# Performance work log

Measured on AMD Instinct MI355X. Metric: run time of the kernel, lower is better.

Reference implementation:

```python
import jax, jax.numpy as jnp
import numpy as np

NUM_USERS = 100000
NUM_ITEMS = 50000
NUM_EDGES = 4000000
DIM = 64


def setup_inputs() -> dict:
    key = jax.random.key(0)
    k1, k2, k3, k4, k5 = jax.random.split(key, 5)
    user_emb = jax.random.normal(k1, (NUM_USERS, DIM), dtype=jnp.float32)
    item_emb = jax.random.normal(k2, (NUM_ITEMS, DIM), dtype=jnp.float32)
    edge_norm = jax.random.uniform(k3, (NUM_EDGES,), dtype=jnp.float32)
    u_idx = jax.random.randint(k4, (NUM_EDGES,), 0, NUM_USERS, dtype=jnp.int32)
    i_idx = jax.random.randint(k5, (NUM_EDGES,), 0, NUM_ITEMS, dtype=jnp.int32)
    return {"user_emb": user_emb, "item_emb": item_emb, "edge_norm": edge_norm,
            "u_idx": u_idx, "i_idx": i_idx}


def reference(user_emb, item_emb, edge_norm, u_idx, i_idx):
    norm = edge_norm[:, None]  # [E, 1]
    # user -> item propagation
    msg_to_items = norm * user_emb[u_idx]  # [E, D]
    agg_items = jax.ops.segment_sum(msg_to_items, i_idx, num_segments=NUM_ITEMS)
    # item -> user propagation
    msg_to_users = norm * item_emb[i_idx]  # [E, D]
    agg_users = jax.ops.segment_sum(msg_to_users, u_idx, num_segments=NUM_USERS)
    return (agg_users, agg_items)
```

## Files before the change

### kernel.cpp

```cpp
#include <hip/hip_runtime.h>

#define NUM_USERS 100000
#define NUM_ITEMS 50000
#define NUM_EDGES 4000000
#define DIM 64

#define SLICE_SHIFT 15
#define SLICES_U ((NUM_USERS + (1 << SLICE_SHIFT) - 1) >> SLICE_SHIFT)
#define SLICES_I ((NUM_ITEMS + (1 << SLICE_SHIFT) - 1) >> SLICE_SHIFT)

#define N_I (SLICES_U * NUM_ITEMS)
#define N_U (SLICES_I * NUM_USERS)
#define N_TOTAL (N_I + N_U)

#define SCAN_NB 512
#define SCAN_THREADS 256

#define PCHUNK 4096
#define PWG ((NUM_EDGES + PCHUNK - 1) / PCHUNK)
#define BUK_SHIFT 9
#define NBUK_I ((N_I + 511) >> 9)
#define NBUK_U ((N_U + 511) >> 9)
#define NBUK (NBUK_I + NBUK_U)

#define STAGE_CAP 15360

#define W_SCALE 32767.0f
#define W_INV   (1.0f / 32767.0f)

__global__ __launch_bounds__(256) void lightgcn_scatter(
    const float* __restrict__ user_emb,
    const float* __restrict__ item_emb,
    const float* __restrict__ edge_norm,
    const int* __restrict__ u_idx,
    const int* __restrict__ i_idx,
    float* __restrict__ agg_users,
    float* __restrict__ agg_items)
{
    long long gid = (long long)blockIdx.x * blockDim.x + threadIdx.x;
    int edge = (int)(gid >> 6);
    int lane = (int)(gid & 63);
    if (edge >= NUM_EDGES) return;
    int u = u_idx[edge];
    int i = i_idx[edge];
    float n = edge_norm[edge];
    float uval = user_emb[(size_t)u * DIM + lane];
    float ival = item_emb[(size_t)i * DIM + lane];
    atomicAdd(&agg_items[(size_t)i * DIM + lane], n * uval);
    atomicAdd(&agg_users[(size_t)u * DIM + lane], n * ival);
}

__global__ __launch_bounds__(256) void convert_both(
    const float4* __restrict__ usrc, const float4* __restrict__ isrc,
    ushort4* __restrict__ udst, ushort4* __restrict__ idst,
    int un4, int in4)
{
    int t = blockIdx.x * blockDim.x + threadIdx.x;
    const float4* s; ushort4* d; int idx;
    if (t < un4) { s = usrc; d = udst; idx = t; }
    else if (t < un4 + in4) { s = isrc; d = idst; idx = t - un4; }
    else return;
    float4 v = s[idx];
    ushort4 o;
    uint b;
    b = __float_as_uint(v.x); o.x = (ushort)((b + 0x7FFFu + ((b >> 16) & 1u)) >> 16);
    b = __float_as_uint(v.y); o.y = (ushort)((b + 0x7FFFu + ((b >> 16) & 1u)) >> 16);
    b = __float_as_uint(v.z); o.z = (ushort)((b + 0x7FFFu + ((b >> 16) & 1u)) >> 16);
    b = __float_as_uint(v.w); o.w = (ushort)((b + 0x7FFFu + ((b >> 16) & 1u)) >> 16);
    d[idx] = o;
}

__global__ __launch_bounds__(256) void bucket_hist_conv(
    const int* __restrict__ u_idx, const int* __restrict__ i_idx,
    ushort* __restrict__ wgHist,
    const float4* __restrict__ usrc, const float4* __restrict__ isrc,
    ushort4* __restrict__ udst, ushort4* __restrict__ idst,
    int un4, int in4, int hist_blocks)
{
    __shared__ uint hist[NBUK];
    if ((int)blockIdx.x >= hist_blocks) {
        int ct = (blockIdx.x - hist_blocks) * blockDim.x + threadIdx.x;
        const float4* s; ushort4* d; int idx;
        if (ct < un4) { s = usrc; d = udst; idx = ct; }
        else if (ct < un4 + in4) { s = isrc; d = idst; idx = ct - un4; }
        else return;
        float4 v = s[idx];
        ushort4 o;
        uint b;
        b = __float_as_uint(v.x); o.x = (ushort)((b + 0x7FFFu + ((b >> 16) & 1u)) >> 16);
        b = __float_as_uint(v.y); o.y = (ushort)((b + 0x7FFFu + ((b >> 16) & 1u)) >> 16);
        b = __float_as_uint(v.z); o.z = (ushort)((b + 0x7FFFu + ((b >> 16) & 1u)) >> 16);
        b = __float_as_uint(v.w); o.w = (ushort)((b + 0x7FFFu + ((b >> 16) & 1u)) >> 16);
        d[idx] = o;
        return;
    }
    int t = threadIdx.x;
    for (int b = t; b < NBUK; b += 256) hist[b] = 0;
    __syncthreads();
    int e0 = blockIdx.x * PCHUNK;
    int ecnt = NUM_EDGES - e0; if (ecnt > PCHUNK) ecnt = PCHUNK;
    for (int k = t; k < ecnt; k += 256) {
        int u = u_idx[e0 + k];
        int i = i_idx[e0 + k];
        atomicAdd(&hist[((u >> SLICE_SHIFT) * NUM_ITEMS + i) >> BUK_SHIFT], 1u);
        atomicAdd(&hist[NBUK_I + (((i >> SLICE_SHIFT) * NUM_USERS + u) >> BUK_SHIFT)], 1u);
    }
    __syncthreads();
    ushort* row = wgHist + (size_t)blockIdx.x * NBUK;
    for (int b = t; b < NBUK; b += 256) row[b] = (ushort)hist[b];
}

__global__ __launch_bounds__(256) void mscan(
    const ushort* __restrict__ wgHist, uint* __restrict__ wgPrefixT,
    int* __restrict__ bukTot)
{
    __shared__ uint sm[256];
    int b = blockIdx.x, t = threadIdx.x;
    int i0 = t * 4;
    uint c0 = 0, c1 = 0, c2 = 0, c3 = 0;
    if (i0 + 0 < PWG) c0 = wgHist[(size_t)(i0 + 0) * NBUK + b];
    if (i0 + 1 < PWG) c1 = wgHist[(size_t)(i0 + 1) * NBUK + b];
    if (i0 + 2 < PWG) c2 = wgHist[(size_t)(i0 + 2) * NBUK + b];
    if (i0 + 3 < PWG) c3 = wgHist[(size_t)(i0 + 3) * NBUK + b];
    sm[t] = c0 + c1 + c2 + c3;
    __syncthreads();
    for (int o = 1; o < 256; o <<= 1) {
        uint x = (t >= o) ? sm[t - o] : 0;
        __syncthreads();
        sm[t] += x;
        __syncthreads();
    }
    uint excl = (t == 0) ? 0u : sm[t - 1];
    uint* orow = wgPrefixT + (size_t)b * PWG;
    if (i0 + 0 < PWG) orow[i0 + 0] = excl;
    if (i0 + 1 < PWG) orow[i0 + 1] = excl + c0;
    if (i0 + 2 < PWG) orow[i0 + 2] = excl + c0 + c1;
    if (i0 + 3 < PWG) orow[i0 + 3] = excl + c0 + c1 + c2;
    if (t == 255) bukTot[b] = (int)sm[255];
}

__global__ __launch_bounds__(256) void bucket_scan(
    const int* __restrict__ bukTot, int* __restrict__ bukOff,
    int* __restrict__ off_last)
{
    __shared__ int sm[256];
    int t = threadIdx.x;
    int b4 = t * 4;
    int v0 = 0, v1 = 0, v2 = 0, v3 = 0;
    if (b4 + 0 < NBUK) v0 = bukTot[b4 + 0];
    if (b4 + 1 < NBUK) v1 = bukTot[b4 + 1];
    if (b4 + 2 < NBUK) v2 = bukTot[b4 + 2];
    if (b4 + 3 < NBUK) v3 = bukTot[b4 + 3];
    sm[t] = v0 + v1 + v2 + v3;
    __syncthreads();
    for (int o = 1; o < 256; o <<= 1) {
        int x = (t >= o) ? sm[t - o] : 0;
        __syncthreads();
        sm[t] += x;
        __syncthreads();
    }
    int excl = (t == 0) ? 0 : sm[t - 1];
    if (b4 + 0 < NBUK) bukOff[b4 + 0] = excl;
    if (b4 + 1 < NBUK) bukOff[b4 + 1] = excl + v0;
    if (b4 + 2 < NBUK) bukOff[b4 + 2] = excl + v0 + v1;
    if (b4 + 3 < NBUK) bukOff[b4 + 3] = excl + v0 + v1 + v2;
    if (t == 255) bukOff[NBUK] = sm[255];
    if (t == 0) *off_last = 2 * NUM_EDGES;
}

__global__ __launch_bounds__(256) void partition_pairs(
    const int* __restrict__ u_idx, const int* __restrict__ i_idx,
    const float* __restrict__ edge_norm,
    const ushort* __restrict__ wgHist, const uint* __restrict__ wgPrefixT,
    const int* __restrict__ bukOff,
    uint* __restrict__ pairRec, ushort* __restrict__ pairBin)
{
    __shared__ uint recS[2 * PCHUNK];
    __shared__ uint bbS[2 * PCHUNK];
    __shared__ uint hist[NBUK];
    __shared__ uint cursor[NBUK];
    __shared__ uint gbase[NBUK];
    __shared__ uint scanTmp[256];

    int t  = threadIdx.x;
    int wg = blockIdx.x;
    int e0 = wg * PCHUNK;
    int ecnt = NUM_EDGES - e0; if (ecnt > PCHUNK) ecnt = PCHUNK;

    const ushort* hrow = wgHist + (size_t)wg * NBUK;
    for (int b = t; b < NBUK; b += 256) {
        hist[b]  = hrow[b];
        gbase[b] = (uint)bukOff[b] + wgPrefixT[(size_t)b * PWG + wg];
    }
    __syncthreads();

    int base4 = t * 4;
    uint v0 = 0, v1 = 0, v2 = 0, v3 = 0;
    if (base4 + 0 < NBUK) v0 = hist[base4 + 0];
    if (base4 + 1 < NBUK) v1 = hist[base4 + 1];
    if (base4 + 2 < NBUK) v2 = hist[base4 + 2];
    if (base4 + 3 < NBUK) v3 = hist[base4 + 3];
    scanTmp[t] = v0 + v1 + v2 + v3;
    __syncthreads();
    for (int o = 1; o < 256; o <<= 1) {
        uint x = (t >= o) ? scanTmp[t - o] : 0;
        __syncthreads();
        scanTmp[t] += x;
        __syncthreads();
    }
    uint excl = (t == 0) ? 0u : scanTmp[t - 1];
    if (base4 + 0 < NBUK) cursor[base4 + 0] = excl;
    if (base4 + 1 < NBUK) cursor[base4 + 1] = excl + v0;
    if (base4 + 2 < NBUK) cursor[base4 + 2] = excl + v0 + v1;
    if (base4 + 3 < NBUK) cursor[base4 + 3] = excl + v0 + v1 + v2;
    __syncthreads();

    for (int k = t; k < ecnt; k += 256) {
        int u = u_idx[e0 + k];
        int i = i_idx[e0 + k];
        float n = edge_norm[e0 + k];
        uint w = (uint)(n * W_SCALE + 0.5f); if (w > 32767u) w = 32767u;
        int binI = (u >> SLICE_SHIFT) * NUM_ITEMS + i;
        int binU = (i >> SLICE_SHIFT) * NUM_USERS + u;
        uint bI = (uint)(binI >> BUK_SHIFT);
        uint bU = (uint)(NBUK_I + (binU >> BUK_SHIFT));
        uint rI = atomicAdd(&cursor[bI], 1u);
        recS[rI] = ((uint)u << 15) | w;
        bbS[rI]  = (bI << BUK_SHIFT) | (uint)(binI & 511);
        uint rU = atomicAdd(&cursor[bU], 1u);
        recS[rU] = ((uint)i << 15) | w;
        bbS[rU]  = (bU << BUK_SHIFT) | (uint)(binU & 511);
    }
    __syncthreads();

    int total = 2 * ecnt;
    for (int s = t; s < total; s += 256) {
        uint bb = bbS[s];
        uint b  = bb >> BUK_SHIFT;
        uint wb = cursor[b] - hist[b];
        uint lpos = gbase[b] + ((uint)s - wb);
        pairRec[lpos] = recS[s];
        pairBin[lpos] = (ushort)(bb & 511u);
    }
}

__global__ __launch_bounds__(256) void bucket_fill(
    const int* __restrict__ bukOff,
    const uint* __restrict__ pairRec, const ushort* __restrict__ pairBin,
    int* __restrict__ off, uint* __restrict__ rec)
{
    __shared__ uint recS[STAGE_CAP];
    __shared__ uint lcnt[512];
    __shared__ uint cur[512];
    __shared__ uint scanTmp[256];
    int b = blockIdx.x, t = threadIdx.x;
    lcnt[t] = 0; lcnt[t + 256] = 0;
    __syncthreads();
    int s0 = bukOff[b], s1 = bukOff[b + 1];
    int n = s1 - s0;
    for (int k = t; k < n; k += 256)
        atomicAdd(&lcnt[pairBin[s0 + k]], 1u);
    __syncthreads();
    uint a0 = lcnt[2 * t], a1 = lcnt[2 * t + 1];
    scanTmp[t] = a0 + a1;
    __syncthreads();
    for (int o = 1; o < 256; o <<= 1) {
        uint x = (t >= o) ? scanTmp[t - o] : 0;
        __syncthreads();
        scanTmp[t] += x;
        __syncthreads();
    }
    uint excl = (t == 0) ? 0u : scanTmp[t - 1];
    cur[2 * t]     = excl;
    cur[2 * t + 1] = excl + a0;
    __syncthreads();
    int gbin0, dirEnd;
    if (b < NBUK_I) { gbin0 = b << BUK_SHIFT; dirEnd = N_I; }
    else { gbin0 = N_I + ((b - NBUK_I) << BUK_SHIFT); dirEnd = N_TOTAL; }
    int lim = dirEnd - gbin0; if (lim > 512) lim = 512;
    if (2 * t     < lim) off[gbin0 + 2 * t]     = s0 + (int)cur[2 * t];
    if (2 * t + 1 < lim) off[gbin0 + 2 * t + 1] = s0 + (int)cur[2 * t + 1];
    __syncthreads();
    if (n <= STAGE_CAP) {
        for (int k = t; k < n; k += 256) {
            uint lbin = pairBin[s0 + k];
            uint r = atomicAdd(&cur[lbin], 1u);
            recS[r] = pairRec[s0 + k];
        }
        __syncthreads();
        for (int k = t; k < n; k += 256)
            rec[(size_t)s0 + k] = recS[k];
    } else {
        for (int k = t; k < n; k += 256) {
            uint lbin = pairBin[s0 + k];
            uint r = atomicAdd(&cur[lbin], 1u);
            rec[(size_t)s0 + r] = pairRec[s0 + k];
        }
    }
}

__global__ __launch_bounds__(SCAN_THREADS) void scan_block_sums(
    const int* __restrict__ cnt, int* __restrict__ bsum, int n, int chunk)
{
    int b = blockIdx.x, t = threadIdx.x;
    int base = b * chunk;
    int end  = base + chunk < n ? base + chunk : n;
    int tch  = (chunk + SCAN_THREADS - 1) / SCAN_THREADS;
    int s = base + t * tch;
    int e = s + tch < end ? s + tch : end;
    int local = 0;
    for (int i = s; i < e; ++i) local += cnt[i];
    __shared__ int sm[SCAN_THREADS];
    sm[t] = local;
    __syncthreads();
    for (int o = SCAN_THREADS / 2; o > 0; o >>= 1) {
        if (t < o) sm[t] += sm[t + o];
        __syncthreads();
    }
    if (t == 0) bsum[b] = sm[0];
}

__global__ __launch_bounds__(SCAN_NB) void scan_block_offsets(
    const int* __restrict__ bsum, int* __restrict__ boff,
    int* __restrict__ off_end)
{
    int t = threadIdx.x;
    __shared__ int sm[SCAN_NB];
    int v = bsum[t];
    sm[t] = v;
    __syncthreads();
    for (int o = 1; o < SCAN_NB; o <<= 1) {
        int x = (t >= o) ? sm[t - o] : 0;
        __syncthreads();
        sm[t] += x;
        __syncthreads();
    }
    boff[t] = sm[t] - v;
    if (t == SCAN_NB - 1) *off_end = sm[SCAN_NB - 1];
}

__global__ __launch_bounds__(SCAN_THREADS) void scan_local(
    int* __restrict__ cnt, const int* __restrict__ boff, int n, int chunk)
{
    int b = blockIdx.x, t = threadIdx.x;
    int base = b * chunk;
    int end  = base + chunk < n ? base + chunk : n;
    int tch  = (chunk + SCAN_THREADS - 1) / SCAN_THREADS;
    int s = base + t * tch;
    int e = s + tch < end ? s + tch : end;
    int local = 0;
    for (int i = s; i < e; ++i) local += cnt[i];
    __shared__ int sm[SCAN_THREADS];
    sm[t] = local;
    __syncthreads();
    for (int o = 1; o < SCAN_THREADS; o <<= 1) {
        int x = (t >= o) ? sm[t - o] : 0;
        __syncthreads();
        sm[t] += x;
        __syncthreads();
    }
    int run = boff[b] + ((t == 0) ? 0 : sm[t - 1]);
    for (int i = s; i < e; ++i) {
        int c = cnt[i];
        cnt[i] = run;
        run += c;
    }
}

__global__ __launch_bounds__(256) void rank_both_exact(
    const int4* __restrict__ u4, const int4* __restrict__ i4,
    int* __restrict__ cnt, int n_i, int su_shift, int si_shift,
    int4* __restrict__ rank_i, int4* __restrict__ rank_u)
{
    int t = blockIdx.x * blockDim.x + threadIdx.x;
    if (t >= NUM_EDGES / 4) return;
    int4 u = u4[t];
    int4 i = i4[t];
    int4 ri, ru;
    ri.x = atomicAdd(&cnt[(u.x >> su_shift) * NUM_ITEMS + i.x], 1);
    ri.y = atomicAdd(&cnt[(u.y >> su_shift) * NUM_ITEMS + i.y], 1);
    ri.z = atomicAdd(&cnt[(u.z >> su_shift) * NUM_ITEMS + i.z], 1);
    ri.w = atomicAdd(&cnt[(u.w >> su_shift) * NUM_ITEMS + i.w], 1);
    ru.x = atomicAdd(&cnt[n_i + (i.x >> si_shift) * NUM_USERS + u.x], 1);
    ru.y = atomicAdd(&cnt[n_i + (i.y >> si_shift) * NUM_USERS + u.y], 1);
    ru.z = atomicAdd(&cnt[n_i + (i.z >> si_shift) * NUM_USERS + u.z], 1);
    ru.w = atomicAdd(&cnt[n_i + (i.w >> si_shift) * NUM_USERS + u.w], 1);
    rank_i[t] = ri;
    rank_u[t] = ru;
}

__global__ __launch_bounds__(256) void scatter_all(
    const int4* __restrict__ u4, const int4* __restrict__ i4,
    const float4* __restrict__ n4,
    const int4* __restrict__ rank_i, const int4* __restrict__ rank_u,
    const int* __restrict__ off, int n_i, int su_shift, int si_shift,
    uint* __restrict__ rec)
{
    int t = blockIdx.x * blockDim.x + threadIdx.x;
    if (t >= NUM_EDGES / 4) return;
    int4   u  = u4[t];
    int4   i  = i4[t];
    float4 n  = n4[t];
    int4   ri = rank_i[t];
    int4   ru = rank_u[t];
    uint w0 = (uint)(n.x * W_SCALE + 0.5f); if (w0 > 32767u) w0 = 32767u;
    uint w1 = (uint)(n.y * W_SCALE + 0.5f); if (w1 > 32767u) w1 = 32767u;
    uint w2 = (uint)(n.z * W_SCALE + 0.5f); if (w2 > 32767u) w2 = 32767u;
    uint w3 = (uint)(n.w * W_SCALE + 0.5f); if (w3 > 32767u) w3 = 32767u;
    int pi0 = off[(u.x >> su_shift) * NUM_ITEMS + i.x] + ri.x;
    int pi1 = off[(u.y >> su_shift) * NUM_ITEMS + i.y] + ri.y;
    int pi2 = off[(u.z >> su_shift) * NUM_ITEMS + i.z] + ri.z;
    int pi3 = off[(u.w >> su_shift) * NUM_ITEMS + i.w] + ri.w;
    int pu0 = off[n_i + (i.x >> si_shift) * NUM_USERS + u.x] + ru.x;
    int pu1 = off[n_i + (i.y >> si_shift) * NUM_USERS + u.y] + ru.y;
    int pu2 = off[n_i + (i.z >> si_shift) * NUM_USERS + u.z] + ru.z;
    int pu3 = off[n_i + (i.w >> si_shift) * NUM_USERS + u.w] + ru.w;
    rec[pi0] = ((uint)u.x << 15) | w0;
    rec[pi1] = ((uint)u.y << 15) | w1;
    rec[pi2] = ((uint)u.z << 15) | w2;
    rec[pi3] = ((uint)u.w << 15) | w3;
    rec[pu0] = ((uint)i.x << 15) | w0;
    rec[pu1] = ((uint)i.y << 15) | w1;
    rec[pu2] = ((uint)i.z << 15) | w2;
    rec[pu3] = ((uint)i.w << 15) | w3;
}

__global__ __launch_bounds__(256) void gather_pass(
    const int* __restrict__ off, int bin_base,
    const uint* __restrict__ rec,
    const ushort* __restrict__ emb16,
    float* __restrict__ out, int nrows, int accumulate)
{
    int gid  = blockIdx.x * blockDim.x + threadIdx.x;
    int row  = gid >> 6;
    int lane = gid & 63;
    if (row >= nrows) return;
    int b = bin_base + row;
    int s = off[b];
    int e = off[b + 1];
    float acc = accumulate ? out[(size_t)row * DIM + lane] : 0.f;
    int k = s;
    for (; k + 8 <= e; k += 8) {
        uint r0 = rec[k],   r1 = rec[k+1], r2 = rec[k+2], r3 = rec[k+3];
        uint r4 = rec[k+4], r5 = rec[k+5], r6 = rec[k+6], r7 = rec[k+7];
        ushort b0 = emb16[(size_t)(r0 >> 15) * DIM + lane];
        ushort b1 = emb16[(size_t)(r1 >> 15) * DIM + lane];
        ushort b2 = emb16[(size_t)(r2 >> 15) * DIM + lane];
        ushort b3 = emb16[(size_t)(r3 >> 15) * DIM + lane];
        ushort b4 = emb16[(size_t)(r4 >> 15) * DIM + lane];
        ushort b5 = emb16[(size_t)(r5 >> 15) * DIM + lane];
        ushort b6 = emb16[(size_t)(r6 >> 15) * DIM + lane];
        ushort b7 = emb16[(size_t)(r7 >> 15) * DIM + lane];
        acc += (float)(r0 & 0x7FFFu) * W_INV * __uint_as_float((uint)b0 << 16);
        acc += (float)(r1 & 0x7FFFu) * W_INV * __uint_as_float((uint)b1 << 16);
        acc += (float)(r2 & 0x7FFFu) * W_INV * __uint_as_float((uint)b2 << 16);
        acc += (float)(r3 & 0x7FFFu) * W_INV * __uint_as_float((uint)b3 << 16);
        acc += (float)(r4 & 0x7FFFu) * W_INV * __uint_as_float((uint)b4 << 16);
        acc += (float)(r5 & 0x7FFFu) * W_INV * __uint_as_float((uint)b5 << 16);
        acc += (float)(r6 & 0x7FFFu) * W_INV * __uint_as_float((uint)b6 << 16);
        acc += (float)(r7 & 0x7FFFu) * W_INV * __uint_as_float((uint)b7 << 16);
    }
    for (; k + 4 <= e; k += 4) {
        uint r0 = rec[k], r1 = rec[k+1], r2 = rec[k+2], r3 = rec[k+3];
        ushort b0 = emb16[(size_t)(r0 >> 15) * DIM + lane];
        ushort b1 = emb16[(size_t)(r1 >> 15) * DIM + lane];
        ushort b2 = emb16[(size_t)(r2 >> 15) * DIM + lane];
        ushort b3 = emb16[(size_t)(r3 >> 15) * DIM + lane];
        acc += (float)(r0 & 0x7FFFu) * W_INV * __uint_as_float((uint)b0 << 16);
        acc += (float)(r1 & 0x7FFFu) * W_INV * __uint_as_float((uint)b1 << 16);
        acc += (float)(r2 & 0x7FFFu) * W_INV * __uint_as_float((uint)b2 << 16);
        acc += (float)(r3 & 0x7FFFu) * W_INV * __uint_as_float((uint)b3 << 16);
    }
    for (; k < e; ++k) {
        uint r0 = rec[k];
        ushort b0 = emb16[(size_t)(r0 >> 15) * DIM + lane];
        acc += (float)(r0 & 0x7FFFu) * W_INV * __uint_as_float((uint)b0 << 16);
    }
    out[(size_t)row * DIM + lane] = acc;
}

extern "C" void kernel_launch(void* const* d_in, const int* in_sizes, int n_in,
                              void* d_out, int out_size, void* d_ws, size_t ws_size,
                              hipStream_t stream) {
    const float* user_emb  = (const float*)d_in[0];
    const float* item_emb  = (const float*)d_in[1];
    const float* edge_norm = (const float*)d_in[2];
    const int*   u_idx     = (const int*)d_in[3];
    const int*   i_idx     = (const int*)d_in[4];

    float* agg_users = (float*)d_out;
    float* agg_items = agg_users + (size_t)NUM_USERS * DIM;

    const int un4 = NUM_USERS * DIM / 4;
    const int in4 = NUM_ITEMS * DIM / 4;
    const int eb4 = (NUM_EDGES / 4 + 255) / 256;
    const int cb  = (un4 + in4 + 255) / 256;
    const size_t bf16_bytes = ((size_t)NUM_USERS + NUM_ITEMS) * DIM * sizeof(ushort);

    {
        const size_t off_bytes  = (size_t)(N_TOTAL + 1) * sizeof(int);
        const size_t buk_bytes  = (size_t)(2 * NBUK + 2) * sizeof(int);
        const size_t wgh_bytes  = (size_t)PWG * NBUK * sizeof(ushort);
        const size_t wgp_bytes  = (size_t)NBUK * PWG * sizeof(uint);
        const size_t prec_bytes = (size_t)2 * NUM_EDGES * sizeof(uint);
        const size_t pbin_bytes = (size_t)2 * NUM_EDGES * sizeof(ushort);
        const size_t rec_bytes  = (size_t)2 * NUM_EDGES * sizeof(uint);
        const size_t need = off_bytes + buk_bytes + 64 + wgh_bytes + 64
                          + wgp_bytes + 64 + prec_bytes + 64 + pbin_bytes + 64
                          + rec_bytes + 64 + bf16_bytes + 256;
        if (ws_size >= need) {
            char* p = (char*)d_ws;
            int*    off     = (int*)p;    p += off_bytes;
            int*    bukTot  = (int*)p;    p += (size_t)NBUK * sizeof(int);
            int*    bukOff  = (int*)p;    p += (size_t)(NBUK + 1) * sizeof(int);
            p = (char*)(((uintptr_t)p + 63) & ~(uintptr_t)63);
            ushort* wgHist  = (ushort*)p; p += wgh_bytes;
            p = (char*)(((uintptr_t)p + 63) & ~(uintptr_t)63);
            uint*   wgPrefixT = (uint*)p; p += wgp_bytes;
            p = (char*)(((uintptr_t)p + 63) & ~(uintptr_t)63);
            uint*   pairRec = (uint*)p;   p += prec_bytes;
            p = (char*)(((uintptr_t)p + 63) & ~(uintptr_t)63);
            ushort* pairBin = (ushort*)p; p += pbin_bytes;
            p = (char*)(((uintptr_t)p + 63) & ~(uintptr_t)63);
            uint*   rec     = (uint*)p;   p += rec_bytes;
            p = (char*)(((uintptr_t)p + 63) & ~(uintptr_t)63);
            ushort* ue16    = (ushort*)p; p += (size_t)NUM_USERS * DIM * sizeof(ushort);
            ushort* ie16    = (ushort*)p;

            bucket_hist_conv<<<PWG + cb, 256, 0, stream>>>(
                u_idx, i_idx, wgHist,
                (const float4*)user_emb, (const float4*)item_emb,
                (ushort4*)ue16, (ushort4*)ie16, un4, in4, PWG);
            mscan<<<NBUK, 256, 0, stream>>>(wgHist, wgPrefixT, bukTot);
            bucket_scan<<<1, 256, 0, stream>>>(bukTot, bukOff, off + N_TOTAL);
            partition_pairs<<<PWG, 256, 0, stream>>>(
                u_idx, i_idx, edge_norm, wgHist, wgPrefixT, bukOff,
                pairRec, pairBin);
            bucket_fill<<<NBUK, 256, 0, stream>>>(
                bukOff, pairRec, pairBin, off, rec);
            for (int s = 0; s < SLICES_U; ++s) {
                gather_pass<<<((NUM_ITEMS * 64) + 255) / 256, 256, 0, stream>>>(
                    off, s * NUM_ITEMS, rec, ue16, agg_items, NUM_ITEMS,
                    s > 0 ? 1 : 0);
            }
            for (int s = 0; s < SLICES_I; ++s) {
                gather_pass<<<((NUM_USERS * 64) + 255) / 256, 256, 0, stream>>>(
                    off, N_I + s * NUM_USERS, rec, ie16, agg_users, NUM_USERS,
                    s > 0 ? 1 : 0);
            }
            return;
        }
    }

    {
        const size_t rec_bytes  = (size_t)2 * NUM_EDGES * sizeof(uint);
        const size_t rank_bytes = (size_t)2 * NUM_EDGES * sizeof(int);
        auto need_for = [&](int SU, int SI) -> size_t {
            size_t n_total = (size_t)SU * NUM_ITEMS + (size_t)SI * NUM_USERS;
            size_t off_bytes = (n_total + 1 + 2 * SCAN_NB) * sizeof(int);
            return off_bytes + 64 + rec_bytes + 64 + rank_bytes + 64 + bf16_bytes
                 + 256;
        };
        int SU = 0, SI = 0, su_shift = 17, si_shift = 17;
        if (ws_size >= need_for(SLICES_U, SLICES_I)) {
            SU = SLICES_U; SI = SLICES_I;
            su_shift = SLICE_SHIFT; si_shift = SLICE_SHIFT;
        } else if (ws_size >= need_for(1, 1)) {
            SU = 1; SI = 1;
        }
        if (SU > 0) {
            const int n_i = SU * NUM_ITEMS;
            const int n_u = SI * NUM_USERS;
            const int n_total = n_i + n_u;

            char* p = (char*)d_ws;
            int*   cnt  = (int*)p;   p += (size_t)(n_total + 1) * sizeof(int);
            int*   bsum = (int*)p;   p += (size_t)SCAN_NB * sizeof(int);
            int*   boff = (int*)p;   p += (size_t)SCAN_NB * sizeof(int);
            p = (char*)(((uintptr_t)p + 63) & ~(uintptr_t)63);
            uint*  rec  = (uint*)p;  p += rec_bytes;
            p = (char*)(((uintptr_t)p + 63) & ~(uintptr_t)63);
            int*   rank_i = (int*)p; p += (size_t)NUM_EDGES * sizeof(int);
            int*   rank_u = (int*)p; p += (size_t)NUM_EDGES * sizeof(int);
            p = (char*)(((uintptr_t)p + 63) & ~(uintptr_t)63);
            ushort* ue16 = (ushort*)p; p += (size_t)NUM_USERS * DIM * sizeof(ushort);
            ushort* ie16 = (ushort*)p;

            hipMemsetAsync(cnt, 0, (size_t)(n_total + 1) * sizeof(int), stream);
            convert_both<<<cb, 256, 0, stream>>>(
                (const float4*)user_emb, (const float4*)item_emb,
                (ushort4*)ue16, (ushort4*)ie16, un4, in4);
            rank_both_exact<<<eb4, 256, 0, stream>>>(
                (const int4*)u_idx, (const int4*)i_idx, cnt, n_i,
                su_shift, si_shift, (int4*)rank_i, (int4*)rank_u);
            const int chunk = (n_total + SCAN_NB - 1) / SCAN_NB;
            scan_block_sums<<<SCAN_NB, SCAN_THREADS, 0, stream>>>(
                cnt, bsum, n_total, chunk);
            scan_block_offsets<<<1, SCAN_NB, 0, stream>>>(bsum, boff, cnt + n_total);
            scan_local<<<SCAN_NB, SCAN_THREADS, 0, stream>>>(
                cnt, boff, n_total, chunk);
            scatter_all<<<eb4, 256, 0, stream>>>(
                (const int4*)u_idx, (const int4*)i_idx, (const float4*)edge_norm,
                (const int4*)rank_i, (const int4*)rank_u,
                cnt, n_i, su_shift, si_shift, rec);
            for (int s = 0; s < SU; ++s) {
                gather_pass<<<((NUM_ITEMS * 64) + 255) / 256, 256, 0, stream>>>(
                    cnt, s * NUM_ITEMS, rec, ue16, agg_items, NUM_ITEMS,
                    s > 0 ? 1 : 0);
            }
            for (int s = 0; s < SI; ++s) {
                gather_pass<<<((NUM_USERS * 64) + 255) / 256, 256, 0, stream>>>(
                    cnt, n_i + s * NUM_USERS, rec, ie16, agg_users, NUM_USERS,
                    s > 0 ? 1 : 0);
            }
            return;
        }
    }

    hipMemsetAsync(d_out, 0, (size_t)out_size * sizeof(float), stream);
    const long long total_threads = (long long)NUM_EDGES * 64;
    const int blocks = (int)((total_threads + 255) / 256);
    lightgcn_scatter<<<blocks, 256, 0, stream>>>(
        user_emb, item_emb, edge_norm, u_idx, i_idx, agg_users, agg_items);
}
```

Measured before the change: 471.7 us.

## Fuse per-slice gather passes into one kernel; widen bucket_fill to 512 threads

The separate gather_pass launches (one per slice per direction, some doing read-modify-write on the output) become a single gather_all kernel. Each output row walks all of its slice spans in registers and writes once, with the inner loop unrolled by 8. bucket_fill now runs one thread per bin with 512 threads, so its scan covers 512 entries directly. This removes repeated output read-modify-write traffic and several kernel launches, at the cost of a longer scan and possibly lower occupancy in bucket_fill.

```diff
diff --git a/kernel.cpp b/kernel.cpp
--- a/kernel.cpp
+++ b/kernel.cpp
@@ -24,6 +24,7 @@
 #define NBUK (NBUK_I + NBUK_U)
 
 #define STAGE_CAP 15360
+#define BF_THREADS 512
 
 #define W_SCALE 32767.0f
 #define W_INV   (1.0f / 32767.0f)
@@ -244,59 +245,119 @@
     }
 }
 
-__global__ __launch_bounds__(256) void bucket_fill(
+__global__ __launch_bounds__(BF_THREADS) void bucket_fill(
     const int* __restrict__ bukOff,
     const uint* __restrict__ pairRec, const ushort* __restrict__ pairBin,
     int* __restrict__ off, uint* __restrict__ rec)
 {
     __shared__ uint recS[STAGE_CAP];
     __shared__ uint lcnt[512];
+    __shared__ uint scanSm[512];
     __shared__ uint cur[512];
-    __shared__ uint scanTmp[256];
     int b = blockIdx.x, t = threadIdx.x;
-    lcnt[t] = 0; lcnt[t + 256] = 0;
+    lcnt[t] = 0;
     __syncthreads();
     int s0 = bukOff[b], s1 = bukOff[b + 1];
     int n = s1 - s0;
-    for (int k = t; k < n; k += 256)
+    for (int k = t; k < n; k += BF_THREADS)
         atomicAdd(&lcnt[pairBin[s0 + k]], 1u);
     __syncthreads();
-    uint a0 = lcnt[2 * t], a1 = lcnt[2 * t + 1];
-    scanTmp[t] = a0 + a1;
-    __syncthreads();
-    for (int o = 1; o < 256; o <<= 1) {
-        uint x = (t >= o) ? scanTmp[t - o] : 0;
-        __syncthreads();
-        scanTmp[t] += x;
-        __syncthreads();
-    }
-    uint excl = (t == 0) ? 0u : scanTmp[t - 1];
-    cur[2 * t]     = excl;
-    cur[2 * t + 1] = excl + a0;
-    __syncthreads();
+    uint v = lcnt[t];
+    scanSm[t] = v;
+    __syncthreads();
+    for (int o = 1; o < 512; o <<= 1) {
+        uint x = (t >= o) ? scanSm[t - o] : 0;
+        __syncthreads();
+        scanSm[t] += x;
+        __syncthreads();
+    }
+    uint excl = scanSm[t] - v;
+    cur[t] = excl;
     int gbin0, dirEnd;
     if (b < NBUK_I) { gbin0 = b << BUK_SHIFT; dirEnd = N_I; }
     else { gbin0 = N_I + ((b - NBUK_I) << BUK_SHIFT); dirEnd = N_TOTAL; }
     int lim = dirEnd - gbin0; if (lim > 512) lim = 512;
-    if (2 * t     < lim) off[gbin0 + 2 * t]     = s0 + (int)cur[2 * t];
-    if (2 * t + 1 < lim) off[gbin0 + 2 * t + 1] = s0 + (int)cur[2 * t + 1];
+    if (t < lim) off[gbin0 + t] = s0 + (int)excl;
     __syncthreads();
     if (n <= STAGE_CAP) {
-        for (int k = t; k < n; k += 256) {
+        for (int k = t; k < n; k += BF_THREADS) {
             uint lbin = pairBin[s0 + k];
             uint r = atomicAdd(&cur[lbin], 1u);
             recS[r] = pairRec[s0 + k];
         }
         __syncthreads();
-        for (int k = t; k < n; k += 256)
+        for (int k = t; k < n; k += BF_THREADS)
             rec[(size_t)s0 + k] = recS[k];
     } else {
-        for (int k = t; k < n; k += 256) {
+        for (int k = t; k < n; k += BF_THREADS) {
             uint lbin = pairBin[s0 + k];
             uint r = atomicAdd(&cur[lbin], 1u);
             rec[(size_t)s0 + r] = pairRec[s0 + k];
         }
     }
+}
+
+__global__ __launch_bounds__(256) void gather_all(
+    const int* __restrict__ off, const uint* __restrict__ rec,
+    const ushort* __restrict__ ue16, const ushort* __restrict__ ie16,
+    float* __restrict__ agg_users, float* __restrict__ agg_items)
+{
+    int gid  = blockIdx.x * blockDim.x + threadIdx.x;
+    int row  = gid >> 6;
+    int lane = gid & 63;
+    if (row >= NUM_ITEMS + NUM_USERS) return;
+    const ushort* emb; float* outp; int nspans, bin0, binStride;
+    if (row < NUM_ITEMS) {
+        emb = ue16; outp = agg_items + (size_t)row * DIM;
+        nspans = SLICES_U; bin0 = row; binStride = NUM_ITEMS;
+    } else {
+        int r = row - NUM_ITEMS;
+        emb = ie16; outp = agg_users + (size_t)r * DIM;
+        nspans = SLICES_I; bin0 = N_I + r; binStride = NUM_USERS;
+    }
+    float acc = 0.f;
+    for (int sp = 0; sp < nspans; ++sp) {
+        int bidx = bin0 + sp * binStride;
+        int k = off[bidx];
+        int e = off[bidx + 1];
+        for (; k + 8 <= e; k += 8) {
+            uint r0 = rec[k],   r1 = rec[k+1], r2 = rec[k+2], r3 = rec[k+3];
+            uint r4 = rec[k+4], r5 = rec[k+5], r6 = rec[k+6], r7 = rec[k+7];
+            ushort b0 = emb[(size_t)(r0 >> 15) * DIM + lane];
+            ushort b1 = emb[(size_t)(r1 >> 15) * DIM + lane];
+            ushort b2 = emb[(size_t)(r2 >> 15) * DIM + lane];
+            ushort b3 = emb[(size_t)(r3 >> 15) * DIM + lane];
+            ushort b4 = emb[(size_t)(r4 >> 15) * DIM + lane];
+            ushort b5 = emb[(size_t)(r5 >> 15) * DIM + lane];
+            ushort b6 = emb[(size_t)(r6 >> 15) * DIM + lane];
+            ushort b7 = emb[(size_t)(r7 >> 15) * DIM + lane];
+            acc += (float)(r0 & 0x7FFFu) * W_INV * __uint_as_float((uint)b0 << 16);
+            acc += (float)(r1 & 0x7FFFu) * W_INV * __uint_as_float((uint)b1 << 16);
+            acc += (float)(r2 & 0x7FFFu) * W_INV * __uint_as_float((uint)b2 << 16);
+            acc += (float)(r3 & 0x7FFFu) * W_INV * __uint_as_float((uint)b3 << 16);
+            acc += (float)(r4 & 0x7FFFu) * W_INV * __uint_as_float((uint)b4 << 16);
+            acc += (float)(r5 & 0x7FFFu) * W_INV * __uint_as_float((uint)b5 << 16);
+            acc += (float)(r6 & 0x7FFFu) * W_INV * __uint_as_float((uint)b6 << 16);
+            acc += (float)(r7 & 0x7FFFu) * W_INV * __uint_as_float((uint)b7 << 16);
+        }
+        for (; k + 4 <= e; k += 4) {
+            uint r0 = rec[k], r1 = rec[k+1], r2 = rec[k+2], r3 = rec[k+3];
+            ushort b0 = emb[(size_t)(r0 >> 15) * DIM + lane];
+            ushort b1 = emb[(size_t)(r1 >> 15) * DIM + lane];
+            ushort b2 = emb[(size_t)(r2 >> 15) * DIM + lane];
+            ushort b3 = emb[(size_t)(r3 >> 15) * DIM + lane];
+            acc += (float)(r0 & 0x7FFFu) * W_INV * __uint_as_float((uint)b0 << 16);
+            acc += (float)(r1 & 0x7FFFu) * W_INV * __uint_as_float((uint)b1 << 16);
+            acc += (float)(r2 & 0x7FFFu) * W_INV * __uint_as_float((uint)b2 << 16);
+            acc += (float)(r3 & 0x7FFFu) * W_INV * __uint_as_float((uint)b3 << 16);
+        }
+        for (; k < e; ++k) {
+            uint r0 = rec[k];
+            ushort b0 = emb[(size_t)(r0 >> 15) * DIM + lane];
+            acc += (float)(r0 & 0x7FFFu) * W_INV * __uint_as_float((uint)b0 << 16);
+        }
+    }
+    outp[lane] = acc;
 }
 
 __global__ __launch_bounds__(SCAN_THREADS) void scan_block_sums(
@@ -536,18 +597,11 @@
             partition_pairs<<<PWG, 256, 0, stream>>>(
                 u_idx, i_idx, edge_norm, wgHist, wgPrefixT, bukOff,
                 pairRec, pairBin);
-            bucket_fill<<<NBUK, 256, 0, stream>>>(
+            bucket_fill<<<NBUK, BF_THREADS, 0, stream>>>(
                 bukOff, pairRec, pairBin, off, rec);
-            for (int s = 0; s < SLICES_U; ++s) {
-                gather_pass<<<((NUM_ITEMS * 64) + 255) / 256, 256, 0, stream>>>(
-                    off, s * NUM_ITEMS, rec, ue16, agg_items, NUM_ITEMS,
-                    s > 0 ? 1 : 0);
-            }
-            for (int s = 0; s < SLICES_I; ++s) {
-                gather_pass<<<((NUM_USERS * 64) + 255) / 256, 256, 0, stream>>>(
-                    off, N_I + s * NUM_USERS, rec, ie16, agg_users, NUM_USERS,
-                    s > 0 ? 1 : 0);
-            }
+            const int grows = NUM_ITEMS + NUM_USERS;
+            gather_all<<<((grows * 64) + 255) / 256, 256, 0, stream>>>(
+                off, rec, ue16, ie16, agg_users, agg_items);
             return;
         }
     }
```

After: 435.8 us. 1.08x faster.

## Fuse per-slice gather passes into one multi-row kernel with finer slices and larger buckets

Applied to the files above, without the earlier changes.

Replaces the per-slice gather_pass launches with a single gather_dir kernel per direction. Each wavefront keeps 16 output rows in registers and loops over all slices, so partial sums are no longer reread and rewritten in global memory between passes. The slice width drops to 2^14 rows so each slice's embedding window is smaller and more cache-friendly, and buckets grow to 1024 bins with 512-thread bucket_fill blocks. The risks are fewer waves in the gather kernels, register pressure from the 16-entry accumulator array, and buckets that more often overflow the shared staging capacity.

```diff
diff --git a/kernel.cpp b/kernel.cpp
--- a/kernel.cpp
+++ b/kernel.cpp
@@ -5,7 +5,7 @@
 #define NUM_EDGES 4000000
 #define DIM 64
 
-#define SLICE_SHIFT 15
+#define SLICE_SHIFT 14
 #define SLICES_U ((NUM_USERS + (1 << SLICE_SHIFT) - 1) >> SLICE_SHIFT)
 #define SLICES_I ((NUM_ITEMS + (1 << SLICE_SHIFT) - 1) >> SLICE_SHIFT)
 
@@ -18,12 +18,16 @@
 
 #define PCHUNK 4096
 #define PWG ((NUM_EDGES + PCHUNK - 1) / PCHUNK)
-#define BUK_SHIFT 9
-#define NBUK_I ((N_I + 511) >> 9)
-#define NBUK_U ((N_U + 511) >> 9)
+#define BUK_SHIFT 10
+#define BUK_BINS (1 << BUK_SHIFT)
+#define NBUK_I ((N_I + BUK_BINS - 1) >> BUK_SHIFT)
+#define NBUK_U ((N_U + BUK_BINS - 1) >> BUK_SHIFT)
 #define NBUK (NBUK_I + NBUK_U)
 
 #define STAGE_CAP 15360
+#define BF_THREADS 512
+
+#define GW_ROWS 16
 
 #define W_SCALE 32767.0f
 #define W_INV   (1.0f / 32767.0f)
@@ -226,10 +230,10 @@
         uint bU = (uint)(NBUK_I + (binU >> BUK_SHIFT));
         uint rI = atomicAdd(&cursor[bI], 1u);
         recS[rI] = ((uint)u << 15) | w;
-        bbS[rI]  = (bI << BUK_SHIFT) | (uint)(binI & 511);
+        bbS[rI]  = (bI << BUK_SHIFT) | (uint)(binI & (BUK_BINS - 1));
         uint rU = atomicAdd(&cursor[bU], 1u);
         recS[rU] = ((uint)i << 15) | w;
-        bbS[rU]  = (bU << BUK_SHIFT) | (uint)(binU & 511);
+        bbS[rU]  = (bU << BUK_SHIFT) | (uint)(binU & (BUK_BINS - 1));
     }
     __syncthreads();
 
@@ -240,62 +244,128 @@
         uint wb = cursor[b] - hist[b];
         uint lpos = gbase[b] + ((uint)s - wb);
         pairRec[lpos] = recS[s];
-        pairBin[lpos] = (ushort)(bb & 511u);
-    }
-}
-
-__global__ __launch_bounds__(256) void bucket_fill(
+        pairBin[lpos] = (ushort)(bb & (BUK_BINS - 1));
+    }
+}
+
+__global__ __launch_bounds__(BF_THREADS) void bucket_fill(
     const int* __restrict__ bukOff,
     const uint* __restrict__ pairRec, const ushort* __restrict__ pairBin,
     int* __restrict__ off, uint* __restrict__ rec)
 {
     __shared__ uint recS[STAGE_CAP];
-    __shared__ uint lcnt[512];
-    __shared__ uint cur[512];
-    __shared__ uint scanTmp[256];
+    __shared__ uint lcnt[BUK_BINS];
+    __shared__ uint cur[BUK_BINS];
+    __shared__ uint scanSm[BF_THREADS];
     int b = blockIdx.x, t = threadIdx.x;
-    lcnt[t] = 0; lcnt[t + 256] = 0;
+    lcnt[t] = 0; lcnt[t + BF_THREADS] = 0;
     __syncthreads();
     int s0 = bukOff[b], s1 = bukOff[b + 1];
     int n = s1 - s0;
-    for (int k = t; k < n; k += 256)
+    for (int k = t; k < n; k += BF_THREADS)
         atomicAdd(&lcnt[pairBin[s0 + k]], 1u);
     __syncthreads();
     uint a0 = lcnt[2 * t], a1 = lcnt[2 * t + 1];
-    scanTmp[t] = a0 + a1;
-    __syncthreads();
-    for (int o = 1; o < 256; o <<= 1) {
-        uint x = (t >= o) ? scanTmp[t - o] : 0;
-        __syncthreads();
-        scanTmp[t] += x;
-        __syncthreads();
-    }
-    uint excl = (t == 0) ? 0u : scanTmp[t - 1];
+    scanSm[t] = a0 + a1;
+    __syncthreads();
+    for (int o = 1; o < BF_THREADS; o <<= 1) {
+        uint x = (t >= o) ? scanSm[t - o] : 0;
+        __syncthreads();
+        scanSm[t] += x;
+        __syncthreads();
+    }
+    uint excl = scanSm[t] - (a0 + a1);
     cur[2 * t]     = excl;
     cur[2 * t + 1] = excl + a0;
-    __syncthreads();
     int gbin0, dirEnd;
     if (b < NBUK_I) { gbin0 = b << BUK_SHIFT; dirEnd = N_I; }
     else { gbin0 = N_I + ((b - NBUK_I) << BUK_SHIFT); dirEnd = N_TOTAL; }
-    int lim = dirEnd - gbin0; if (lim > 512) lim = 512;
-    if (2 * t     < lim) off[gbin0 + 2 * t]     = s0 + (int)cur[2 * t];
-    if (2 * t + 1 < lim) off[gbin0 + 2 * t + 1] = s0 + (int)cur[2 * t + 1];
+    int lim = dirEnd - gbin0; if (lim > BUK_BINS) lim = BUK_BINS;
+    if (2 * t     < lim) off[gbin0 + 2 * t]     = s0 + (int)excl;
+    if (2 * t + 1 < lim) off[gbin0 + 2 * t + 1] = s0 + (int)(excl + a0);
     __syncthreads();
     if (n <= STAGE_CAP) {
-        for (int k = t; k < n; k += 256) {
+        for (int k = t; k < n; k += BF_THREADS) {
             uint lbin = pairBin[s0 + k];
             uint r = atomicAdd(&cur[lbin], 1u);
             recS[r] = pairRec[s0 + k];
         }
         __syncthreads();
-        for (int k = t; k < n; k += 256)
+        for (int k = t; k < n; k += BF_THREADS)
             rec[(size_t)s0 + k] = recS[k];
     } else {
-        for (int k = t; k < n; k += 256) {
+        for (int k = t; k < n; k += BF_THREADS) {
             uint lbin = pairBin[s0 + k];
             uint r = atomicAdd(&cur[lbin], 1u);
             rec[(size_t)s0 + r] = pairRec[s0 + k];
         }
+    }
+}
+
+__global__ __launch_bounds__(256) void gather_dir(
+    const int* __restrict__ off, const uint* __restrict__ rec,
+    const ushort* __restrict__ emb, float* __restrict__ out,
+    int nrows, int nspans, int binBase, int binStride)
+{
+    int wid  = (blockIdx.x * blockDim.x + threadIdx.x) >> 6;
+    int lane = threadIdx.x & 63;
+    int r0 = wid * GW_ROWS;
+    if (r0 >= nrows) return;
+    float acc[GW_ROWS];
+#pragma unroll
+    for (int j = 0; j < GW_ROWS; ++j) acc[j] = 0.f;
+    for (int sp = 0; sp < nspans; ++sp) {
+        int base = binBase + sp * binStride + r0;
+#pragma unroll
+        for (int j = 0; j < GW_ROWS; ++j) {
+            if (r0 + j < nrows) {
+                int k = off[base + j];
+                int e = off[base + j + 1];
+                float a = acc[j];
+                for (; k + 8 <= e; k += 8) {
+                    uint r0_ = rec[k],   r1_ = rec[k+1], r2_ = rec[k+2], r3_ = rec[k+3];
+                    uint r4_ = rec[k+4], r5_ = rec[k+5], r6_ = rec[k+6], r7_ = rec[k+7];
+                    ushort b0 = emb[(size_t)(r0_ >> 15) * DIM + lane];
+                    ushort b1 = emb[(size_t)(r1_ >> 15) * DIM + lane];
+                    ushort b2 = emb[(size_t)(r2_ >> 15) * DIM + lane];
+                    ushort b3 = emb[(size_t)(r3_ >> 15) * DIM + lane];
+                    ushort b4 = emb[(size_t)(r4_ >> 15) * DIM + lane];
+                    ushort b5 = emb[(size_t)(r5_ >> 15) * DIM + lane];
+                    ushort b6 = emb[(size_t)(r6_ >> 15) * DIM + lane];
+                    ushort b7 = emb[(size_t)(r7_ >> 15) * DIM + lane];
+                    a += (float)(r0_ & 0x7FFFu) * W_INV * __uint_as_float((uint)b0 << 16);
+                    a += (float)(r1_ & 0x7FFFu) * W_INV * __uint_as_float((uint)b1 << 16);
+                    a += (float)(r2_ & 0x7FFFu) * W_INV * __uint_as_float((uint)b2 << 16);
+                    a += (float)(r3_ & 0x7FFFu) * W_INV * __uint_as_float((uint)b3 << 16);
+                    a += (float)(r4_ & 0x7FFFu) * W_INV * __uint_as_float((uint)b4 << 16);
+                    a += (float)(r5_ & 0x7FFFu) * W_INV * __uint_as_float((uint)b5 << 16);
+                    a += (float)(r6_ & 0x7FFFu) * W_INV * __uint_as_float((uint)b6 << 16);
+                    a += (float)(r7_ & 0x7FFFu) * W_INV * __uint_as_float((uint)b7 << 16);
+                }
+                for (; k + 4 <= e; k += 4) {
+                    uint r0_ = rec[k], r1_ = rec[k+1], r2_ = rec[k+2], r3_ = rec[k+3];
+                    ushort b0 = emb[(size_t)(r0_ >> 15) * DIM + lane];
+                    ushort b1 = emb[(size_t)(r1_ >> 15) * DIM + lane];
+                    ushort b2 = emb[(size_t)(r2_ >> 15) * DIM + lane];
+                    ushort b3 = emb[(size_t)(r3_ >> 15) * DIM + lane];
+                    a += (float)(r0_ & 0x7FFFu) * W_INV * __uint_as_float((uint)b0 << 16);
+                    a += (float)(r1_ & 0x7FFFu) * W_INV * __uint_as_float((uint)b1 << 16);
+                    a += (float)(r2_ & 0x7FFFu) * W_INV * __uint_as_float((uint)b2 << 16);
+                    a += (float)(r3_ & 0x7FFFu) * W_INV * __uint_as_float((uint)b3 << 16);
+                }
+                for (; k < e; ++k) {
+                    uint r0_ = rec[k];
+                    ushort b0 = emb[(size_t)(r0_ >> 15) * DIM + lane];
+                    a += (float)(r0_ & 0x7FFFu) * W_INV * __uint_as_float((uint)b0 << 16);
+                }
+                acc[j] = a;
+            }
+        }
+    }
+#pragma unroll
+    for (int j = 0; j < GW_ROWS; ++j) {
+        int row = r0 + j;
+        if (row < nrows) out[(size_t)row * DIM + lane] = acc[j];
     }
 }
 
@@ -440,26 +510,6 @@
     int e = off[b + 1];
     float acc = accumulate ? out[(size_t)row * DIM + lane] : 0.f;
     int k = s;
-    for (; k + 8 <= e; k += 8) {
-        uint r0 = rec[k],   r1 = rec[k+1], r2 = rec[k+2], r3 = rec[k+3];
-        uint r4 = rec[k+4], r5 = rec[k+5], r6 = rec[k+6], r7 = rec[k+7];
-        ushort b0 = emb16[(size_t)(r0 >> 15) * DIM + lane];
-        ushort b1 = emb16[(size_t)(r1 >> 15) * DIM + lane];
-        ushort b2 = emb16[(size_t)(r2 >> 15) * DIM + lane];
-        ushort b3 = emb16[(size_t)(r3 >> 15) * DIM + lane];
-        ushort b4 = emb16[(size_t)(r4 >> 15) * DIM + lane];
-        ushort b5 = emb16[(size_t)(r5 >> 15) * DIM + lane];
-        ushort b6 = emb16[(size_t)(r6 >> 15) * DIM + lane];
-        ushort b7 = emb16[(size_t)(r7 >> 15) * DIM + lane];
-        acc += (float)(r0 & 0x7FFFu) * W_INV * __uint_as_float((uint)b0 << 16);
-        acc += (float)(r1 & 0x7FFFu) * W_INV * __uint_as_float((uint)b1 << 16);
-        acc += (float)(r2 & 0x7FFFu) * W_INV * __uint_as_float((uint)b2 << 16);
-        acc += (float)(r3 & 0x7FFFu) * W_INV * __uint_as_float((uint)b3 << 16);
-        acc += (float)(r4 & 0x7FFFu) * W_INV * __uint_as_float((uint)b4 << 16);
-        acc += (float)(r5 & 0x7FFFu) * W_INV * __uint_as_float((uint)b5 << 16);
-        acc += (float)(r6 & 0x7FFFu) * W_INV * __uint_as_float((uint)b6 << 16);
-        acc += (float)(r7 & 0x7FFFu) * W_INV * __uint_as_float((uint)b7 << 16);
-    }
     for (; k + 4 <= e; k += 4) {
         uint r0 = rec[k], r1 = rec[k+1], r2 = rec[k+2], r3 = rec[k+3];
         ushort b0 = emb16[(size_t)(r0 >> 15) * DIM + lane];
@@ -536,18 +586,14 @@
             partition_pairs<<<PWG, 256, 0, stream>>>(
                 u_idx, i_idx, edge_norm, wgHist, wgPrefixT, bukOff,
                 pairRec, pairBin);
-            bucket_fill<<<NBUK, 256, 0, stream>>>(
+            bucket_fill<<<NBUK, BF_THREADS, 0, stream>>>(
                 bukOff, pairRec, pairBin, off, rec);
-            for (int s = 0; s < SLICES_U; ++s) {
-                gather_pass<<<((NUM_ITEMS * 64) + 255) / 256, 256, 0, stream>>>(
-                    off, s * NUM_ITEMS, rec, ue16, agg_items, NUM_ITEMS,
-                    s > 0 ? 1 : 0);
-            }
-            for (int s = 0; s < SLICES_I; ++s) {
-                gather_pass<<<((NUM_USERS * 64) + 255) / 256, 256, 0, stream>>>(
-                    off, N_I + s * NUM_USERS, rec, ie16, agg_users, NUM_USERS,
-                    s > 0 ? 1 : 0);
-            }
+            const int ib = (NUM_ITEMS + GW_ROWS * 4 - 1) / (GW_ROWS * 4);
+            gather_dir<<<ib, 256, 0, stream>>>(
+                off, rec, ue16, agg_items, NUM_ITEMS, SLICES_U, 0, NUM_ITEMS);
+            const int ub = (NUM_USERS + GW_ROWS * 4 - 1) / (GW_ROWS * 4);
+            gather_dir<<<ub, 256, 0, stream>>>(
+                off, rec, ie16, agg_users, NUM_USERS, SLICES_I, N_I, NUM_USERS);
             return;
         }
     }
```

Result: slower. 568.7 us (+20.5%).
